# Kernel optimization log

Hardware: AMD Instinct MI355X
Metric: run time of the kernel (lower is better)

## Reference

```python
import jax, jax.numpy as jnp
import numpy as np

B, C, H, W = 8, 48, 256, 256
N_PROMPTS = 16
N_EXPERTS = 8
N_GROUPS = 4
TOP_K = 2
GROUP_DIM = C // N_GROUPS
DN = ('NCHW', 'OIHW', 'NCHW')


def _conv(x, w, groups=1, pad=0):
    return jax.lax.conv_general_dilated(
        x, w, window_strides=(1, 1), padding=[(pad, pad), (pad, pad)],
        dimension_numbers=DN, feature_group_count=groups)


def setup_inputs() -> dict:
    key = jax.random.key(0)
    ks = jax.random.split(key, 10)
    s = 0.02
    return {
        'x': jax.random.normal(ks[0], (B, C, H, W), jnp.float32),
        'P_hat': jax.random.normal(ks[1], (B, N_PROMPTS, C), jnp.float32),
        'proj_a_w': jax.random.normal(ks[2], (C, C, 1, 1), jnp.float32) * s,
        'proj_b_w': jax.random.normal(ks[3], (C, C, 1, 1), jnp.float32) * s,
        'dw_b_w': jax.random.normal(ks[4], (C, 1, 3, 3), jnp.float32) * s,
        'fi_align_w': jax.random.normal(ks[5], (C, N_GROUPS, 1, 1), jnp.float32) * s,
        'expert_w1': jax.random.normal(ks[6], (N_EXPERTS, C, C, 3, 3), jnp.float32) * s,
        'expert_w2': jax.random.normal(ks[7], (N_EXPERTS, C, C, 3, 3), jnp.float32) * s,
        'router_w': jax.random.normal(ks[8], (N_EXPERTS, C), jnp.float32) * s,
        'router_b': jax.random.normal(ks[9], (N_EXPERTS,), jnp.float32) * s,
    }


def reference(x, P_hat, proj_a_w, proj_b_w, dw_b_w, fi_align_w,
              expert_w1, expert_w2, router_w, router_b):
    b, c, h, w = x.shape
    # branch a: 1x1 proj + group-wise prompt-conditioned filter activation
    xa = _conv(x, proj_a_w)                               # [B,C,H,W]
    p_avg = P_hat.mean(axis=1)                            # [B,C]
    xa_g = xa.reshape(b, N_GROUPS, GROUP_DIM, h * w)      # [B,G,gd,HW]
    p_g = p_avg.reshape(b, N_GROUPS, GROUP_DIM)           # [B,G,gd]
    fi = jnp.einsum('bgc,bgcn->bgn', p_g, xa_g)           # [B,G,HW]
    fi = fi.reshape(b, N_GROUPS, h, w)
    fi = _conv(fi, fi_align_w)                            # [B,C,H,W]
    # branch b: 1x1 proj + depthwise 3x3
    xb = _conv(_conv(x, proj_b_w), dw_b_w, groups=c, pad=1)
    Fx = xb + fi
    # routing: GAP -> linear -> top-k softmax gate
    gap = Fx.mean(axis=(2, 3))                            # [B,C]
    scores = gap @ router_w.T + router_b                  # [B,E]
    topk_val, topk_idx = jax.lax.top_k(scores, TOP_K)
    gate = jnp.zeros_like(scores).at[
        jnp.arange(b)[:, None], topk_idx
    ].set(jax.nn.softmax(topk_val, axis=-1))              # [B,E]
    # experts: dense compute then weighted sum (matches dense-then-mask math)
    out = jnp.zeros_like(Fx)
    for i in range(N_EXPERTS):
        hmid = jax.nn.gelu(_conv(Fx, expert_w1[i], pad=1), approximate=False)
        e_out = _conv(hmid, expert_w2[i], pad=1)
        out = out + gate[:, i][:, None, None, None] * e_out
    return out + x
```

## Files before the change

kernel.cpp:

```cpp
#include <hip/hip_runtime.h>
#include <hip/hip_bf16.h>
#include <math.h>

#define BATCH 8
#define CH 48
#define HH 256
#define WW 256
#define NPROMPT 16
#define NEXP 8
#define NGRP 4
#define GDIM 12
#define HW (HH * WW)

#define FRAG_ELEMS (9 * 3 * 2 * 64 * 8)
#define FRAG_BYTES (FRAG_ELEMS * 2)

typedef short bf16x8 __attribute__((ext_vector_type(8)));
typedef float f32x4  __attribute__((ext_vector_type(4)));
typedef unsigned short u16x4 __attribute__((ext_vector_type(4)));

#define TILE 16
#define ITILE 18
#define NPIX (ITILE * ITILE)
#define PIXB 128
#define LDSPIX 328
#define LDSBYTES (LDSPIX * PIXB)
#define GPIXB 96
#define IMGB ((size_t)HW * GPIXB)

__device__ __forceinline__ unsigned short f2bf(float f) {
    unsigned u = __float_as_uint(f);
    unsigned r = (u + 0x7FFFu + ((u >> 16) & 1u)) >> 16;
    return (unsigned short)r;
}

__device__ __forceinline__ void load_lds16(const void* g, void* l) {
    __builtin_amdgcn_global_load_lds(
        (const __attribute__((address_space(1))) unsigned int*)g,
        (__attribute__((address_space(3))) unsigned int*)l, 16, 0, 0);
}

__global__ __launch_bounds__(256) void precompute_kernel(
    const float* __restrict__ P_hat,
    const float* __restrict__ proj_a_w,
    const float* __restrict__ proj_b_w,
    const float* __restrict__ dw_b_w,
    const float* __restrict__ fi_align_w,
    unsigned short* __restrict__ wfxf,
    float* __restrict__ zpage)
{
    int b = blockIdx.x;
    int tid = threadIdx.x;
    __shared__ float p_avg[CH];
    __shared__ float W_fi[NGRP * CH];
    __shared__ float W_a[CH * CH];

    if (tid < CH) {
        float s = 0.f;
        for (int n = 0; n < NPROMPT; n++)
            s += P_hat[(b * NPROMPT + n) * CH + tid];
        p_avg[tid] = s * (1.0f / NPROMPT);
    }
    if (b == 0 && tid < 64) zpage[tid] = 0.f;
    __syncthreads();

    if (tid < NGRP * CH) {
        int g = tid / CH, k = tid % CH;
        float s = 0.f;
        for (int j = 0; j < GDIM; j++) {
            int c = g * GDIM + j;
            s += p_avg[c] * proj_a_w[c * CH + k];
        }
        W_fi[tid] = s;
    }
    __syncthreads();

    for (int e = tid; e < CH * CH; e += 256) {
        int o = e / CH, k = e % CH;
        float s = 0.f;
        for (int g = 0; g < NGRP; g++)
            s += fi_align_w[o * NGRP + g] * W_fi[g * CH + k];
        W_a[e] = s;
    }
    __syncthreads();

    for (int i = tid; i < FRAG_ELEMS; i += 256) {
        int j = i & 7;
        int lane = (i >> 3) & 63;
        int blk = i >> 9;
        int kb = blk & 1;
        int tmp = blk >> 1;
        int mt = tmp % 3, tap = tmp / 3;
        int oc = mt * 16 + (lane & 15);
        int cin = kb * 32 + (lane >> 4) * 8 + j;
        float v = 0.f;
        if (cin < CH) {
            v = dw_b_w[oc * 9 + tap] * proj_b_w[oc * CH + cin];
            if (tap == 4) v += W_a[oc * CH + cin];
        }
        wfxf[(size_t)b * FRAG_ELEMS + i] = f2bf(v);
    }
}

__global__ __launch_bounds__(256) void repack_kernel(
    const float* __restrict__ w1, const float* __restrict__ w2,
    unsigned short* __restrict__ w1f, unsigned short* __restrict__ w2f)
{
    int e = blockIdx.x;
    const float* src = blockIdx.y ? w2 : w1;
    unsigned short* dst = blockIdx.y ? w2f : w1f;
    for (int i = threadIdx.x; i < FRAG_ELEMS; i += 256) {
        int j = i & 7;
        int lane = (i >> 3) & 63;
        int blk = i >> 9;
        int kb = blk & 1;
        int tmp = blk >> 1;
        int mt = tmp % 3, tap = tmp / 3;
        int oc = mt * 16 + (lane & 15);
        int cin = kb * 32 + (lane >> 4) * 8 + j;
        float v = (cin < CH) ? src[(((size_t)e * CH + oc) * CH + cin) * 9 + tap] : 0.f;
        dst[(size_t)e * FRAG_ELEMS + i] = f2bf(v);
    }
}

__global__ __launch_bounds__(256) void transpose_kernel(
    const float* __restrict__ x, unsigned short* __restrict__ xT)
{
    __shared__ float t[CH * 65];
    int pix0 = blockIdx.x * 64;
    int b = pix0 >> 16;
    int rem = pix0 & 65535;
    int tid = threadIdx.x;
    int px = tid & 63, c0 = tid >> 6;

    float v[12];
#pragma unroll
    for (int k = 0; k < 12; k++)
        v[k] = x[(((size_t)(b * CH + c0 + 4 * k)) << 16) + rem + px];
#pragma unroll
    for (int k = 0; k < 12; k++)
        t[(c0 + 4 * k) * 65 + px] = v[k];
    __syncthreads();

#pragma unroll
    for (int k = 0; k < 2; k++) {
        int w = tid + 256 * k;
        if (w < 384) {
            int p2 = w / 6, o = w % 6;
            bf16x8 pk;
#pragma unroll
            for (int j = 0; j < 8; j++)
                pk[j] = (short)f2bf(t[(o * 8 + j) * 65 + p2]);
            *(bf16x8*)((char*)xT + (size_t)pix0 * GPIXB + (size_t)w * 16) = pk;
        }
    }
}

__device__ __forceinline__ void stage_swz(
    const char* __restrict__ srcimg, int oy0, int ox0,
    char* smem, const char* __restrict__ zp)
{
    int wv = threadIdx.x >> 6, lane = threadIdx.x & 63;
    for (int k = wv; k < 41; k += 4) {
        int w = k * 64 + lane;
        int px = w >> 3, o = w & 7;
        int yy = px / ITILE, xx = px - yy * ITILE;
        int gy = oy0 + yy - 1, gx = ox0 + xx - 1;
        int m = o ^ (gx & 7);
        const char* g = zp;
        if (px < NPIX && (unsigned)gy < 256u && (unsigned)gx < 256u && m < 6)
            g = srcimg + (size_t)((gy << 8) + gx) * GPIXB + m * 16;
        load_lds16(g, smem + k * 1024);
    }
}

template <bool ACC>
__device__ __forceinline__ void conv_core(
    const char* smem, const unsigned short* __restrict__ wfrag,
    int ox0, f32x4 acc[4][3])
{
    const int lane = threadIdx.x & 63;
    const int wv = threadIdx.x >> 6;
    const int n = lane & 15;
    const int quad = lane >> 4;
    const bf16x8* wp = (const bf16x8*)wfrag;

    if (!ACC) {
#pragma unroll
        for (int g = 0; g < 4; ++g)
#pragma unroll
            for (int mt = 0; mt < 3; ++mt)
                acc[g][mt] = (f32x4){0.f, 0.f, 0.f, 0.f};
    }

    int colb0[3], colb1[3];
#pragma unroll
    for (int dx = 0; dx < 3; ++dx) {
        int key = (ox0 - 1 + dx + n) & 7;
        colb0[dx] = (dx + n) * PIXB + ((quad ^ key) * 16);
        colb1[dx] = (dx + n) * PIXB + (((quad + 4) ^ key) * 16);
    }

    bf16x8 a[2][6];
#pragma unroll
    for (int mt = 0; mt < 3; ++mt) {
        a[0][mt]     = wp[(mt * 2 + 0) * 64 + lane];
        a[0][mt + 3] = wp[(mt * 2 + 1) * 64 + lane];
    }

#pragma unroll
    for (int tap = 0; tap < 9; ++tap) {
        const int cur = tap & 1;
        if (tap < 8) {
#pragma unroll
            for (int mt = 0; mt < 3; ++mt) {
                a[cur ^ 1][mt]     = wp[(((tap + 1) * 3 + mt) * 2 + 0) * 64 + lane];
                a[cur ^ 1][mt + 3] = wp[(((tap + 1) * 3 + mt) * 2 + 1) * 64 + lane];
            }
        }
        const int dy = tap / 3, dx = tap % 3;
#pragma unroll
        for (int g = 0; g < 4; ++g) {
            const int rowb = (wv * 4 + g + dy) * (ITILE * PIXB);
            bf16x8 b0 = *(const bf16x8*)(smem + rowb + colb0[dx]);
            bf16x8 b1 = *(const bf16x8*)(smem + rowb + colb1[dx]);
            acc[g][0] = __builtin_amdgcn_mfma_f32_16x16x32_bf16(a[cur][0], b0, acc[g][0], 0, 0, 0);
            acc[g][1] = __builtin_amdgcn_mfma_f32_16x16x32_bf16(a[cur][1], b0, acc[g][1], 0, 0, 0);
            acc[g][2] = __builtin_amdgcn_mfma_f32_16x16x32_bf16(a[cur][2], b0, acc[g][2], 0, 0, 0);
            acc[g][0] = __builtin_amdgcn_mfma_f32_16x16x32_bf16(a[cur][3], b1, acc[g][0], 0, 0, 0);
            acc[g][1] = __builtin_amdgcn_mfma_f32_16x16x32_bf16(a[cur][4], b1, acc[g][1], 0, 0, 0);
            acc[g][2] = __builtin_amdgcn_mfma_f32_16x16x32_bf16(a[cur][5], b1, acc[g][2], 0, 0, 0);
        }
    }
}

__device__ __forceinline__ void store_pix(
    char* __restrict__ dstimg, int row, int col, int quad,
    const f32x4 v[3])
{
    size_t pb = (size_t)((row << 8) + col) * GPIXB;
#pragma unroll
    for (int mt = 0; mt < 3; ++mt) {
        u16x4 pk;
#pragma unroll
        for (int r = 0; r < 4; ++r) pk[r] = f2bf(v[mt][r]);
        *(u16x4*)(dstimg + pb + mt * 32 + quad * 8) = pk;
    }
}

__global__ __launch_bounds__(256, 3) void fxconv_kernel(
    const unsigned short* __restrict__ xT, const unsigned short* __restrict__ wfxf,
    unsigned short* __restrict__ Fx, float* __restrict__ gapP,
    const float* __restrict__ zp)
{
    __shared__ __align__(16) char smem[LDSBYTES];
    int ox0 = blockIdx.x * TILE, oy0 = blockIdx.y * TILE, b = blockIdx.z;

    stage_swz((const char*)xT + (size_t)b * IMGB, oy0, ox0, smem, (const char*)zp);
    __syncthreads();

    f32x4 acc[4][3];
    conv_core<false>(smem, wfxf + (size_t)b * FRAG_ELEMS, ox0, acc);

    const int lane = threadIdx.x & 63;
    const int wv = threadIdx.x >> 6;
    const int n = lane & 15, quad = lane >> 4;
    char* dimg = (char*)Fx + (size_t)b * IMGB;

    float gsum[3][4];
#pragma unroll
    for (int mt = 0; mt < 3; ++mt)
#pragma unroll
        for (int r = 0; r < 4; ++r) gsum[mt][r] = 0.f;

#pragma unroll
    for (int g = 0; g < 4; ++g) {
        int row = oy0 + wv * 4 + g;
        store_pix(dimg, row, ox0 + n, quad, acc[g]);
#pragma unroll
        for (int mt = 0; mt < 3; ++mt)
#pragma unroll
            for (int r = 0; r < 4; ++r) gsum[mt][r] += acc[g][mt][r];
    }
#pragma unroll
    for (int mt = 0; mt < 3; ++mt)
#pragma unroll
        for (int r = 0; r < 4; ++r) {
            float v = gsum[mt][r];
            v += __shfl_xor(v, 1);
            v += __shfl_xor(v, 2);
            v += __shfl_xor(v, 4);
            v += __shfl_xor(v, 8);
            gsum[mt][r] = v;
        }

    __syncthreads();
    float* smemf = (float*)smem;
    if (n == 0) {
#pragma unroll
        for (int mt = 0; mt < 3; ++mt)
#pragma unroll
            for (int r = 0; r < 4; ++r)
                smemf[wv * CH + mt * 16 + quad * 4 + r] = gsum[mt][r];
    }
    __syncthreads();
    int t = threadIdx.x;
    if (t < CH) {
        float v = smemf[t] + smemf[CH + t] + smemf[2 * CH + t] + smemf[3 * CH + t];
        int tile = blockIdx.y * 16 + blockIdx.x;
        gapP[((size_t)b * 256 + tile) * CH + t] = v;
    }
}

__global__ __launch_bounds__(256) void route_kernel(
    const float* __restrict__ gapP,
    const float* __restrict__ router_w,
    const float* __restrict__ router_b,
    float* __restrict__ gate, int* __restrict__ eidx)
{
    __shared__ float red4[4 * CH];
    __shared__ float scs[NEXP];
    int b = blockIdx.x, t = threadIdx.x;
    int lane = t & 63, wv = t >> 6;

    const float* src = gapP + ((size_t)b * 256 + t) * CH;
    float s[CH];
#pragma unroll
    for (int c = 0; c < CH; c++) s[c] = src[c];
#pragma unroll
    for (int c = 0; c < CH; c++) {
        float v = s[c];
        v += __shfl_xor(v, 1);
        v += __shfl_xor(v, 2);
        v += __shfl_xor(v, 4);
        v += __shfl_xor(v, 8);
        v += __shfl_xor(v, 16);
        v += __shfl_xor(v, 32);
        if (lane == 0) red4[wv * CH + c] = v;
    }
    __syncthreads();

    if (t < NEXP) {
        float sc = router_b[t];
        for (int c = 0; c < CH; c++) {
            float g = (red4[c] + red4[CH + c] + red4[2 * CH + c] + red4[3 * CH + c])
                      * (1.0f / HW);
            sc += g * router_w[t * CH + c];
        }
        scs[t] = sc;
    }
    __syncthreads();

    if (t == 0) {
        float v0 = -1e30f, v1 = -1e30f;
        int i0 = 0, i1 = 0;
        for (int e = 0; e < NEXP; e++) {
            float se = scs[e];
            if (se > v0) { v1 = v0; i1 = i0; v0 = se; i0 = e; }
            else if (se > v1) { v1 = se; i1 = e; }
        }
        float ex = expf(v1 - v0);
        float dn = 1.0f / (1.0f + ex);
        gate[b * 2 + 0] = dn;
        gate[b * 2 + 1] = ex * dn;
        eidx[b * 2 + 0] = i0;
        eidx[b * 2 + 1] = i1;
    }
}

__global__ __launch_bounds__(256) void scale_kernel(
    const unsigned short* __restrict__ w2f, const float* __restrict__ gate,
    const int* __restrict__ eidx, unsigned short* __restrict__ w2s)
{
    int b = blockIdx.x, s = blockIdx.y;
    int e = eidx[b * 2 + s];
    float g = gate[b * 2 + s];
    const unsigned short* src = w2f + (size_t)e * FRAG_ELEMS;
    unsigned short* dst = w2s + (size_t)(b * 2 + s) * FRAG_ELEMS;
    for (int i = threadIdx.x; i < FRAG_ELEMS; i += 256) {
        float v = __uint_as_float((unsigned)src[i] << 16);
        dst[i] = f2bf(v * g);
    }
}

__global__ __launch_bounds__(256, 3) void conv1_both_kernel(
    const unsigned short* __restrict__ Fx, const unsigned short* __restrict__ w1f,
    const int* __restrict__ eidx, const float* __restrict__ zp,
    unsigned short* __restrict__ hmid0, unsigned short* __restrict__ hmid1)
{
    __shared__ __align__(16) char smem[LDSBYTES];
    int ox0 = blockIdx.x * TILE, oy0 = blockIdx.y * TILE, b = blockIdx.z;

    stage_swz((const char*)Fx + (size_t)b * IMGB, oy0, ox0, smem, (const char*)zp);
    __syncthreads();

    const int lane = threadIdx.x & 63;
    const int wv = threadIdx.x >> 6;
    const int n = lane & 15, quad = lane >> 4;

    f32x4 acc[4][3];
#pragma unroll
    for (int s = 0; s < 2; ++s) {
        int e = __builtin_amdgcn_readfirstlane(eidx[b * 2 + s]);
        conv_core<false>(smem, w1f + (size_t)e * FRAG_ELEMS, ox0, acc);
        char* dimg = (char*)(s ? hmid1 : hmid0) + (size_t)b * IMGB;
#pragma unroll
        for (int g = 0; g < 4; ++g) {
            int row = oy0 + wv * 4 + g;
            f32x4 h[3];
#pragma unroll
            for (int mt = 0; mt < 3; ++mt)
#pragma unroll
                for (int r = 0; r < 4; ++r) {
                    float a = acc[g][mt][r];
                    h[mt][r] = 0.5f * a * (1.0f + erff(a * 0.70710678118654752f));
                }
            store_pix(dimg, row, ox0 + n, quad, h);
        }
    }
}

__global__ __launch_bounds__(256, 3) void conv2_both_kernel(
    const unsigned short* __restrict__ hmid0, const unsigned short* __restrict__ hmid1,
    const unsigned short* __restrict__ w2s, const float* __restrict__ zp,
    const float* __restrict__ x, float* __restrict__ out)
{
    __shared__ __align__(16) char smem[LDSBYTES];
    int ox0 = blockIdx.x * TILE, oy0 = blockIdx.y * TILE, b = blockIdx.z;

    f32x4 acc[4][3];

    stage_swz((const char*)hmid0 + (size_t)b * IMGB, oy0, ox0, smem, (const char*)zp);
    __syncthreads();
    conv_core<false>(smem, w2s + (size_t)(b * 2 + 0) * FRAG_ELEMS, ox0, acc);
    __syncthreads();

    stage_swz((const char*)hmid1 + (size_t)b * IMGB, oy0, ox0, smem, (const char*)zp);
    __syncthreads();
    conv_core<true>(smem, w2s + (size_t)(b * 2 + 1) * FRAG_ELEMS, ox0, acc);

    const int lane = threadIdx.x & 63;
    const int wv = threadIdx.x >> 6;
    const int n = lane & 15, quad = lane >> 4;
#pragma unroll
    for (int g = 0; g < 4; ++g) {
        int row = oy0 + wv * 4 + g;
#pragma unroll
        for (int mt = 0; mt < 3; ++mt)
#pragma unroll
            for (int r = 0; r < 4; ++r) {
                int oc = mt * 16 + quad * 4 + r;
                size_t idx = (((size_t)b * CH + oc) << 16) + (row << 8) + ox0 + n;
                out[idx] = x[idx] + acc[g][mt][r];
            }
    }
}

extern "C" void kernel_launch(void* const* d_in, const int* in_sizes, int n_in,
                              void* d_out, int out_size, void* d_ws, size_t ws_size,
                              hipStream_t stream) {
    (void)in_sizes; (void)n_in; (void)out_size; (void)ws_size;
    const float* x          = (const float*)d_in[0];
    const float* P_hat      = (const float*)d_in[1];
    const float* proj_a_w   = (const float*)d_in[2];
    const float* proj_b_w   = (const float*)d_in[3];
    const float* dw_b_w     = (const float*)d_in[4];
    const float* fi_align_w = (const float*)d_in[5];
    const float* expert_w1  = (const float*)d_in[6];
    const float* expert_w2  = (const float*)d_in[7];
    const float* router_w   = (const float*)d_in[8];
    const float* router_b   = (const float*)d_in[9];
    float* out = (float*)d_out;

    char* ob = (char*)d_out;
    unsigned short* Fx   = (unsigned short*)ob;
    unsigned short* wfxf = (unsigned short*)(ob + 62914560);
    unsigned short* w1f  = (unsigned short*)(ob + 62914560 + FRAG_BYTES * NEXP);
    unsigned short* w2f  = (unsigned short*)(ob + 62914560 + 2 * FRAG_BYTES * NEXP);
    float*          gapP = (float*)(ob + 64241664);

    char* ws = (char*)d_ws;
    unsigned short* xT    = (unsigned short*)ws;
    unsigned short* hmid1 = (unsigned short*)ws;
    unsigned short* hmid0 = (unsigned short*)(ws + 50331648);
    unsigned short* w2s   = (unsigned short*)(ws + 100663296);
    float* zp   = (float*)(ws + 100663296 + 884736);
    float* gate = (float*)(ws + 100663296 + 884736 + 256 + 1536);
    int*   eidx = (int*)(gate + BATCH * 2);

    precompute_kernel<<<dim3(BATCH), 256, 0, stream>>>(
        P_hat, proj_a_w, proj_b_w, dw_b_w, fi_align_w, wfxf, zp);

    repack_kernel<<<dim3(NEXP, 2), 256, 0, stream>>>(
        expert_w1, expert_w2, w1f, w2f);

    transpose_kernel<<<dim3(BATCH * HW / 64), 256, 0, stream>>>(x, xT);

    fxconv_kernel<<<dim3(16, 16, BATCH), 256, 0, stream>>>(xT, wfxf, Fx, gapP, zp);

    route_kernel<<<dim3(BATCH), 256, 0, stream>>>(gapP, router_w, router_b, gate, eidx);

    scale_kernel<<<dim3(BATCH, 2), 256, 0, stream>>>(w2f, gate, eidx, w2s);

    conv1_both_kernel<<<dim3(16, 16, BATCH), 256, 0, stream>>>(
        Fx, w1f, eidx, zp, hmid0, hmid1);

    conv2_both_kernel<<<dim3(16, 16, BATCH), 256, 0, stream>>>(
        hmid0, hmid1, w2s, zp, x, out);
}
```

Before: 537.7 us.

## Stage per-wave halo rows, replace barriers with vmcnt waits, vectorize residual epilogue

LDS staging is reorganized so each wave loads only the six halo rows it consumes into its own region. That lets the block-wide __syncthreads after staging be replaced by a per-wave s_waitcnt vmcnt(0). In conv2, the MFMA operands are swapped so the accumulator layout puts four consecutive pixels per lane, and the residual read and output write become 16-byte vector accesses. The x residual loads are also hoisted before the convolutions so their latency overlaps the staging. The cost is duplicated halo loads between waves (more global traffic, slightly larger LDS) and reliance on wave-local DMA completion for correctness.

Result: slower. 598.0 us (+11.2%).

```diff
diff --git a/kernel.cpp b/kernel.cpp
--- a/kernel.cpp
+++ b/kernel.cpp
@@ -23,8 +23,8 @@
 #define ITILE 18
 #define NPIX (ITILE * ITILE)
 #define PIXB 128
-#define LDSPIX 328
-#define LDSBYTES (LDSPIX * PIXB)
+#define ROWB (ITILE * PIXB)
+#define LDSBYTES 41984
 #define GPIXB 96
 #define IMGB ((size_t)HW * GPIXB)
 
@@ -156,25 +156,33 @@
     }
 }
 
-__device__ __forceinline__ void stage_swz(
+__device__ __forceinline__ void stage_rows(
     const char* __restrict__ srcimg, int oy0, int ox0,
     char* smem, const char* __restrict__ zp)
 {
     int wv = threadIdx.x >> 6, lane = threadIdx.x & 63;
-    for (int k = wv; k < 41; k += 4) {
+    char* base = smem + wv * (4 * ROWB);
+#pragma unroll
+    for (int k = 0; k < 14; ++k) {
         int w = k * 64 + lane;
-        int px = w >> 3, o = w & 7;
-        int yy = px / ITILE, xx = px - yy * ITILE;
-        int gy = oy0 + yy - 1, gx = ox0 + xx - 1;
+        int rl = w / 144;
+        int idx = w - rl * 144;
+        int px = idx >> 3, o = idx & 7;
+        int tr = wv * 4 + rl;
+        int gy = oy0 + tr - 1, gx = ox0 + px - 1;
         int m = o ^ (gx & 7);
         const char* g = zp;
-        if (px < NPIX && (unsigned)gy < 256u && (unsigned)gx < 256u && m < 6)
+        if ((unsigned)gy < 256u && (unsigned)gx < 256u && m < 6)
             g = srcimg + (size_t)((gy << 8) + gx) * GPIXB + m * 16;
-        load_lds16(g, smem + k * 1024);
-    }
-}
-
-template <bool ACC>
+        load_lds16(g, base + k * 1024);
+    }
+}
+
+__device__ __forceinline__ void wait_dma() {
+    asm volatile("s_waitcnt vmcnt(0)" ::: "memory");
+}
+
+template <bool ACC, bool SWAP>
 __device__ __forceinline__ void conv_core(
     const char* smem, const unsigned short* __restrict__ wfrag,
     int ox0, f32x4 acc[4][3])
@@ -221,15 +229,24 @@
         const int dy = tap / 3, dx = tap % 3;
 #pragma unroll
         for (int g = 0; g < 4; ++g) {
-            const int rowb = (wv * 4 + g + dy) * (ITILE * PIXB);
+            const int rowb = (wv * 4 + g + dy) * ROWB;
             bf16x8 b0 = *(const bf16x8*)(smem + rowb + colb0[dx]);
             bf16x8 b1 = *(const bf16x8*)(smem + rowb + colb1[dx]);
-            acc[g][0] = __builtin_amdgcn_mfma_f32_16x16x32_bf16(a[cur][0], b0, acc[g][0], 0, 0, 0);
-            acc[g][1] = __builtin_amdgcn_mfma_f32_16x16x32_bf16(a[cur][1], b0, acc[g][1], 0, 0, 0);
-            acc[g][2] = __builtin_amdgcn_mfma_f32_16x16x32_bf16(a[cur][2], b0, acc[g][2], 0, 0, 0);
-            acc[g][0] = __builtin_amdgcn_mfma_f32_16x16x32_bf16(a[cur][3], b1, acc[g][0], 0, 0, 0);
-            acc[g][1] = __builtin_amdgcn_mfma_f32_16x16x32_bf16(a[cur][4], b1, acc[g][1], 0, 0, 0);
-            acc[g][2] = __builtin_amdgcn_mfma_f32_16x16x32_bf16(a[cur][5], b1, acc[g][2], 0, 0, 0);
+            if (SWAP) {
+                acc[g][0] = __builtin_amdgcn_mfma_f32_16x16x32_bf16(b0, a[cur][0], acc[g][0], 0, 0, 0);
+                acc[g][1] = __builtin_amdgcn_mfma_f32_16x16x32_bf16(b0, a[cur][1], acc[g][1], 0, 0, 0);
+                acc[g][2] = __builtin_amdgcn_mfma_f32_16x16x32_bf16(b0, a[cur][2], acc[g][2], 0, 0, 0);
+                acc[g][0] = __builtin_amdgcn_mfma_f32_16x16x32_bf16(b1, a[cur][3], acc[g][0], 0, 0, 0);
+                acc[g][1] = __builtin_amdgcn_mfma_f32_16x16x32_bf16(b1, a[cur][4], acc[g][1], 0, 0, 0);
+                acc[g][2] = __builtin_amdgcn_mfma_f32_16x16x32_bf16(b1, a[cur][5], acc[g][2], 0, 0, 0);
+            } else {
+                acc[g][0] = __builtin_amdgcn_mfma_f32_16x16x32_bf16(a[cur][0], b0, acc[g][0], 0, 0, 0);
+                acc[g][1] = __builtin_amdgcn_mfma_f32_16x16x32_bf16(a[cur][1], b0, acc[g][1], 0, 0, 0);
+                acc[g][2] = __builtin_amdgcn_mfma_f32_16x16x32_bf16(a[cur][2], b0, acc[g][2], 0, 0, 0);
+                acc[g][0] = __builtin_amdgcn_mfma_f32_16x16x32_bf16(a[cur][3], b1, acc[g][0], 0, 0, 0);
+                acc[g][1] = __builtin_amdgcn_mfma_f32_16x16x32_bf16(a[cur][4], b1, acc[g][1], 0, 0, 0);
+                acc[g][2] = __builtin_amdgcn_mfma_f32_16x16x32_bf16(a[cur][5], b1, acc[g][2], 0, 0, 0);
+            }
         }
     }
 }
@@ -256,11 +273,11 @@
     __shared__ __align__(16) char smem[LDSBYTES];
     int ox0 = blockIdx.x * TILE, oy0 = blockIdx.y * TILE, b = blockIdx.z;
 
-    stage_swz((const char*)xT + (size_t)b * IMGB, oy0, ox0, smem, (const char*)zp);
-    __syncthreads();
+    stage_rows((const char*)xT + (size_t)b * IMGB, oy0, ox0, smem, (const char*)zp);
+    wait_dma();
 
     f32x4 acc[4][3];
-    conv_core<false>(smem, wfxf + (size_t)b * FRAG_ELEMS, ox0, acc);
+    conv_core<false, false>(smem, wfxf + (size_t)b * FRAG_ELEMS, ox0, acc);
 
     const int lane = threadIdx.x & 63;
     const int wv = threadIdx.x >> 6;
@@ -391,8 +408,8 @@
     __shared__ __align__(16) char smem[LDSBYTES];
     int ox0 = blockIdx.x * TILE, oy0 = blockIdx.y * TILE, b = blockIdx.z;
 
-    stage_swz((const char*)Fx + (size_t)b * IMGB, oy0, ox0, smem, (const char*)zp);
-    __syncthreads();
+    stage_rows((const char*)Fx + (size_t)b * IMGB, oy0, ox0, smem, (const char*)zp);
+    wait_dma();
 
     const int lane = threadIdx.x & 63;
     const int wv = threadIdx.x >> 6;
@@ -402,7 +419,7 @@
 #pragma unroll
     for (int s = 0; s < 2; ++s) {
         int e = __builtin_amdgcn_readfirstlane(eidx[b * 2 + s]);
-        conv_core<false>(smem, w1f + (size_t)e * FRAG_ELEMS, ox0, acc);
+        conv_core<false, false>(smem, w1f + (size_t)e * FRAG_ELEMS, ox0, acc);
         char* dimg = (char*)(s ? hmid1 : hmid0) + (size_t)b * IMGB;
 #pragma unroll
         for (int g = 0; g < 4; ++g) {
@@ -428,31 +445,42 @@
     __shared__ __align__(16) char smem[LDSBYTES];
     int ox0 = blockIdx.x * TILE, oy0 = blockIdx.y * TILE, b = blockIdx.z;
 
-    f32x4 acc[4][3];
-
-    stage_swz((const char*)hmid0 + (size_t)b * IMGB, oy0, ox0, smem, (const char*)zp);
-    __syncthreads();
-    conv_core<false>(smem, w2s + (size_t)(b * 2 + 0) * FRAG_ELEMS, ox0, acc);
-    __syncthreads();
-
-    stage_swz((const char*)hmid1 + (size_t)b * IMGB, oy0, ox0, smem, (const char*)zp);
-    __syncthreads();
-    conv_core<true>(smem, w2s + (size_t)(b * 2 + 1) * FRAG_ELEMS, ox0, acc);
-
     const int lane = threadIdx.x & 63;
     const int wv = threadIdx.x >> 6;
     const int n = lane & 15, quad = lane >> 4;
+
+    f32x4 xr[4][3];
 #pragma unroll
     for (int g = 0; g < 4; ++g) {
         int row = oy0 + wv * 4 + g;
 #pragma unroll
-        for (int mt = 0; mt < 3; ++mt)
-#pragma unroll
-            for (int r = 0; r < 4; ++r) {
-                int oc = mt * 16 + quad * 4 + r;
-                size_t idx = (((size_t)b * CH + oc) << 16) + (row << 8) + ox0 + n;
-                out[idx] = x[idx] + acc[g][mt][r];
-            }
+        for (int nt = 0; nt < 3; ++nt) {
+            int oc = nt * 16 + n;
+            size_t idx = (((size_t)b * CH + oc) << 16) + (row << 8) + ox0 + quad * 4;
+            xr[g][nt] = *(const f32x4*)(x + idx);
+        }
+    }
+
+    f32x4 acc[4][3];
+
+    stage_rows((const char*)hmid0 + (size_t)b * IMGB, oy0, ox0, smem, (const char*)zp);
+    wait_dma();
+    conv_core<false, true>(smem, w2s + (size_t)(b * 2 + 0) * FRAG_ELEMS, ox0, acc);
+    __syncthreads();
+
+    stage_rows((const char*)hmid1 + (size_t)b * IMGB, oy0, ox0, smem, (const char*)zp);
+    wait_dma();
+    conv_core<true, true>(smem, w2s + (size_t)(b * 2 + 1) * FRAG_ELEMS, ox0, acc);
+
+#pragma unroll
+    for (int g = 0; g < 4; ++g) {
+        int row = oy0 + wv * 4 + g;
+#pragma unroll
+        for (int nt = 0; nt < 3; ++nt) {
+            int oc = nt * 16 + n;
+            size_t idx = (((size_t)b * CH + oc) << 16) + (row << 8) + ox0 + quad * 4;
+            *(f32x4*)(out + idx) = xr[g][nt] + acc[g][nt];
+        }
     }
 }
 
```
